# Performance work log

Measured on AMD Instinct MI355X. Metric: run time of the kernel, lower is better.

Reference implementation:

```python
import jax, jax.numpy as jnp
import numpy as np

B, T, I, H, O = 8192, 128, 28, 200, 10


def setup_inputs() -> dict:
    key = jax.random.key(0)
    ks = jax.random.split(key, 7)
    s_ih = 1.0 / np.sqrt(H)
    return {
        "x": jax.random.normal(ks[0], (B, T, I), dtype=jnp.float32),
        "W_ih": jax.random.uniform(ks[1], (H, I), jnp.float32, -s_ih, s_ih),
        "W_hh": jax.random.uniform(ks[2], (H, H), jnp.float32, -s_ih, s_ih),
        "b_ih": jax.random.uniform(ks[3], (H,), jnp.float32, -s_ih, s_ih),
        "b_hh": jax.random.uniform(ks[4], (H,), jnp.float32, -s_ih, s_ih),
        "W_fc": jax.random.uniform(ks[5], (O, H), jnp.float32, -s_ih, s_ih),
        "b_fc": jax.random.uniform(ks[6], (O,), jnp.float32, -s_ih, s_ih),
    }


def reference(x, W_ih, W_hh, b_ih, b_hh, W_fc, b_fc):
    # Precompute input projections for all timesteps in one GEMM: [B,T,H]
    xp = jnp.einsum("bti,hi->bth", x, W_ih) + b_ih + b_hh
    h0 = jnp.zeros((x.shape[0], W_hh.shape[0]), dtype=x.dtype)

    def step(h, xp_t):
        # h_t = relu(x_t W_ih^T + b_ih + h_{t-1} W_hh^T + b_hh)
        h = jax.nn.relu(xp_t + h @ W_hh.T)
        return h, None

    # scan over time: xp transposed to [T,B,H]
    h_last, _ = jax.lax.scan(step, h0, jnp.swapaxes(xp, 0, 1))
    # out[:, -1, :] then fc1
    return h_last @ W_fc.T + b_fc
```

## Files before the change

kernel.cpp:

```cpp
#include <hip/hip_runtime.h>

typedef float f4v __attribute__((ext_vector_type(4)));
typedef short s8v __attribute__((ext_vector_type(8)));

#define TT 128
#define II 28
#define HH 200
#define BB 16
#define NT 512
#define CH 8
#define KX 224
#define NCH (TT / CH)

template <bool B> struct BC { static constexpr bool value = B; };

__device__ __forceinline__ unsigned pk_hu(float a, float b) {
    unsigned ua = __builtin_bit_cast(unsigned, a) + 0x8000u;
    unsigned ub = __builtin_bit_cast(unsigned, b) + 0x8000u;
    return __builtin_amdgcn_perm(ub, ua, 0x07060302);
}
__device__ __forceinline__ short f2bf(float f) {
    return (short)((__builtin_bit_cast(unsigned, f) + 0x8000u) >> 16);
}
__device__ __forceinline__ float bf2f(short s) {
    return __builtin_bit_cast(float, ((unsigned)(unsigned short)s) << 16);
}

#define STEP_BAR() asm volatile("s_waitcnt lgkmcnt(0)\n\ts_barrier" ::: "memory")
#define VSTEP_BAR() asm volatile("s_waitcnt vmcnt(0) lgkmcnt(0)\n\ts_barrier" ::: "memory")

__global__ __launch_bounds__(NT, 4)
void rnn_r13(const float* __restrict__ x,
             const float* __restrict__ W_ih,
             const float* __restrict__ W_hh,
             const float* __restrict__ b_ih,
             const float* __restrict__ b_hh,
             const float* __restrict__ W_fc,
             const float* __restrict__ b_fc,
             float* __restrict__ out)
{
    __shared__ __align__(16) short Hf[2][7][512];
    __shared__ __align__(16) short Xf[2][CH][512];
    __shared__ __align__(16) float Xl[CH * BB * II];

    const int tid  = threadIdx.x;
    const int lane = tid & 63;
    const int q    = lane >> 4;
    const int lr   = lane & 15;
    const int wave = __builtin_amdgcn_readfirstlane(tid >> 6);
    const int b0   = blockIdx.x * BB;

    const bool two = (wave < 5);
    const int jt0  = two ? 2 * wave : 10 + (wave - 5);
    const int jt1  = two ? 2 * wave + 1 : 13;

    const int nIss = (wave < 6) ? 2 : 1;
    const int e0   = (wave < 6) ? 2 * wave : 12 + (wave - 6);
    unsigned xoff[2];
    #pragma unroll
    for (int k = 0; k < 2; ++k) {
        const int e  = e0 + k;
        const int m  = (e << 6) + lane;
        const int tl = m / 112;
        const int rm = m - tl * 112;
        const int r  = rm / 7;
        const int c4 = rm - r * 7;
        xoff[k] = (unsigned)(((((b0 + r) * TT + tl) * II) + c4 * 4) * 4);
    }
    auto issue_dma = [&](int c) {
        #pragma unroll
        for (int k = 0; k < 2; ++k) {
            if (k < nIss) {
                const char* src = (const char*)x + (xoff[k] + (unsigned)c * (CH * II * 4));
                float* dst = &Xl[(e0 + k) * 256];
                __builtin_amdgcn_global_load_lds(
                    (const __attribute__((address_space(1))) void*)src,
                    (__attribute__((address_space(3))) void*)dst, 16, 0, 0);
            }
        }
    };

    auto prepass = [&](int tc) {
        if (tid < 448) {
            const f4v v0 = *(const f4v*)&Xl[tid * 8];
            const f4v v1 = *(const f4v*)&Xl[tid * 8 + 4];
            const unsigned d[4] = { pk_hu(v0.x, v0.y), pk_hu(v0.z, v0.w),
                                    pk_hu(v1.x, v1.y), pk_hu(v1.z, v1.w) };
            int* dstb = ((int*)Xf) + (tc & 1) * 2048;
            #pragma unroll
            for (int dk = 0; dk < 4; ++dk) {
                const int kk = tid * 4 + dk;
                const int t  = kk / 224;
                const int k2 = kk - t * 224;
                const int r  = k2 / 14;
                const int cp = k2 - r * 14;
                dstb[t * 256 + 64 * (cp >> 2) + 4 * r + (cp & 3)] = (int)d[dk];
            }
        }
    };

    issue_dma(0);

    s8v Af[2][8];
    #pragma unroll
    for (int u = 0; u < 2; ++u) {
        const int j = 16 * (u ? jt1 : jt0) + lr;
        #pragma unroll
        for (int kc = 0; kc < 8; ++kc) {
            union { short s[8]; s8v v; } tv;
            #pragma unroll
            for (int i = 0; i < 8; ++i) {
                const int k = 32 * kc + 8 * q + i;
                float w = 0.0f;
                if (j < HH) {
                    if (k < HH)                     w = W_hh[j * HH + k];
                    else if (k >= KX && k < KX+II)  w = W_ih[j * II + (k - KX)];
                    else if (k == KX + II) {
                        w = b_ih[j] + b_hh[j];
                    } else if (k == KX + II + 1) {
                        const float bs = b_ih[j] + b_hh[j];
                        w = bs - bf2f(f2bf(bs));
                    }
                }
                tv.s[i] = f2bf(w);
            }
            Af[u][kc] = tv.v;
        }
    }

    for (int i = tid; i < 2 * 7 * 512 / 2; i += NT) ((int*)Hf)[i] = 0;
    for (int i = tid; i < 2 * CH * 512 / 2; i += NT)
        ((int*)Xf)[i] = (((i & 255) >= 194) && ((i & 3) == 2)) ? 0x3f803f80 : 0;

    const int j0w = 16 * jt0 + 4 * q;
    short* st0 = &Hf[0][j0w >> 5][(16 * ((j0w >> 3) & 3) + lr) * 8 + (j0w & 7)];
    const int j1w = 16 * jt1 + 4 * q;
    short* st1 = &Hf[0][j1w >> 5][(16 * ((j1w >> 3) & 3) + lr) * 8 + (j1w & 7)];
    const int HFH = 7 * 512;

    __syncthreads();
    prepass(0);
    STEP_BAR();
    issue_dma(1);

    if ((blockIdx.x >> 8) & 1) asm volatile("s_sleep 23");

    const f4v Z = {0.f, 0.f, 0.f, 0.f};
    f4v a0, a1;

    {
        const s8v xb = *(const s8v*)&Xf[0][0][lane * 8];
        a0 = __builtin_amdgcn_mfma_f32_16x16x32_bf16(Af[0][7], xb, Z, 0, 0, 0);
        if (two) a1 = __builtin_amdgcn_mfma_f32_16x16x32_bf16(Af[1][7], xb, Z, 0, 0, 0);
    }
    STEP_BAR();

    auto chunk = [&](int c, auto TWOC) {
        constexpr bool TWO = decltype(TWOC)::value;
        #pragma unroll
        for (int s = 0; s < CH; ++s) {
            const int pb = s & 1;
            const short* hf = &Hf[pb][0][lane * 8];
            if constexpr (TWO) {
                s8v g0 = *(const s8v*)(hf);
                s8v g1 = *(const s8v*)(hf + 512);
                s8v g2 = *(const s8v*)(hf + 1024);
                s8v g3 = *(const s8v*)(hf + 1536);
                a0 = __builtin_amdgcn_mfma_f32_16x16x32_bf16(Af[0][0], g0, a0, 0, 0, 0);
                a1 = __builtin_amdgcn_mfma_f32_16x16x32_bf16(Af[1][0], g0, a1, 0, 0, 0);
                g0 = *(const s8v*)(hf + 2048);
                a0 = __builtin_amdgcn_mfma_f32_16x16x32_bf16(Af[0][1], g1, a0, 0, 0, 0);
                a1 = __builtin_amdgcn_mfma_f32_16x16x32_bf16(Af[1][1], g1, a1, 0, 0, 0);
                g1 = *(const s8v*)(hf + 2560);
                a0 = __builtin_amdgcn_mfma_f32_16x16x32_bf16(Af[0][2], g2, a0, 0, 0, 0);
                a1 = __builtin_amdgcn_mfma_f32_16x16x32_bf16(Af[1][2], g2, a1, 0, 0, 0);
                g2 = *(const s8v*)(hf + 3072);
                a0 = __builtin_amdgcn_mfma_f32_16x16x32_bf16(Af[0][3], g3, a0, 0, 0, 0);
                a1 = __builtin_amdgcn_mfma_f32_16x16x32_bf16(Af[1][3], g3, a1, 0, 0, 0);
                a0 = __builtin_amdgcn_mfma_f32_16x16x32_bf16(Af[0][4], g0, a0, 0, 0, 0);
                a1 = __builtin_amdgcn_mfma_f32_16x16x32_bf16(Af[1][4], g0, a1, 0, 0, 0);
                a0 = __builtin_amdgcn_mfma_f32_16x16x32_bf16(Af[0][5], g1, a0, 0, 0, 0);
                a1 = __builtin_amdgcn_mfma_f32_16x16x32_bf16(Af[1][5], g1, a1, 0, 0, 0);
                a0 = __builtin_amdgcn_mfma_f32_16x16x32_bf16(Af[0][6], g2, a0, 0, 0, 0);
                a1 = __builtin_amdgcn_mfma_f32_16x16x32_bf16(Af[1][6], g2, a1, 0, 0, 0);
            } else {
                s8v g0 = *(const s8v*)(hf);
                s8v g1 = *(const s8v*)(hf + 1536);
                s8v g2 = *(const s8v*)(hf + 2048);
                s8v g3 = *(const s8v*)(hf + 2560);
                a1 = __builtin_amdgcn_mfma_f32_16x16x32_bf16(Af[0][3], g1, Z, 0, 0, 0);
                g1 = *(const s8v*)(hf + 512);
                a0 = __builtin_amdgcn_mfma_f32_16x16x32_bf16(Af[0][0], g0, a0, 0, 0, 0);
                g0 = *(const s8v*)(hf + 1024);
                a1 = __builtin_amdgcn_mfma_f32_16x16x32_bf16(Af[0][4], g2, a1, 0, 0, 0);
                g2 = *(const s8v*)(hf + 3072);
                a0 = __builtin_amdgcn_mfma_f32_16x16x32_bf16(Af[0][1], g1, a0, 0, 0, 0);
                a1 = __builtin_amdgcn_mfma_f32_16x16x32_bf16(Af[0][5], g3, a1, 0, 0, 0);
                a0 = __builtin_amdgcn_mfma_f32_16x16x32_bf16(Af[0][2], g0, a0, 0, 0, 0);
                a1 = __builtin_amdgcn_mfma_f32_16x16x32_bf16(Af[0][6], g2, a1, 0, 0, 0);
            }
            {
                const int wo = (pb ^ 1) * HFH;
                int2 hv;
                if constexpr (!TWO) a0 += a1;
                hv.x = (int)pk_hu(fmaxf(a0.x, 0.f), fmaxf(a0.y, 0.f));
                hv.y = (int)pk_hu(fmaxf(a0.z, 0.f), fmaxf(a0.w, 0.f));
                *(int2*)(st0 + wo) = hv;
                if constexpr (TWO) {
                    hv.x = (int)pk_hu(fmaxf(a1.x, 0.f), fmaxf(a1.y, 0.f));
                    hv.y = (int)pk_hu(fmaxf(a1.z, 0.f), fmaxf(a1.w, 0.f));
                    *(int2*)(st1 + wo) = hv;
                }
            }
            if (s < CH - 1) {
                const s8v xb = *(const s8v*)&Xf[c & 1][s + 1][lane * 8];
                a0 = __builtin_amdgcn_mfma_f32_16x16x32_bf16(Af[0][7], xb, Z, 0, 0, 0);
                if constexpr (TWO)
                    a1 = __builtin_amdgcn_mfma_f32_16x16x32_bf16(Af[1][7], xb, Z, 0, 0, 0);
            } else if (c + 1 < NCH) {
                const s8v xb = *(const s8v*)&Xf[(c + 1) & 1][0][lane * 8];
                a0 = __builtin_amdgcn_mfma_f32_16x16x32_bf16(Af[0][7], xb, Z, 0, 0, 0);
                if constexpr (TWO)
                    a1 = __builtin_amdgcn_mfma_f32_16x16x32_bf16(Af[1][7], xb, Z, 0, 0, 0);
            }
            if (s == 4 && c + 1 < NCH) prepass(c + 1);
            if (s == 5 && c + 2 < NCH) issue_dma(c + 2);
            if (s == 3) VSTEP_BAR();
            else        STEP_BAR();
        }
    };

    #pragma unroll 1
    for (int c = 0; c < NCH; ++c) {
        if (two) chunk(c, BC<true>{});
        else     chunk(c, BC<false>{});
    }

    __syncthreads();
    if (tid < BB * 10) {
        const int o = tid >> 4, r = tid & 15;
        const float* wrow = W_fc + o * HH;
        float acc = b_fc[o];
        #pragma unroll 1
        for (int kb = 0; kb < 25; ++kb) {
            const s8v hv = *(const s8v*)&Hf[0][kb >> 2][(16 * (kb & 3) + r) * 8];
            const f4v w0 = *(const f4v*)(wrow + kb * 8);
            const f4v w1 = *(const f4v*)(wrow + kb * 8 + 4);
            acc = fmaf(bf2f(hv[0]), w0.x, acc);
            acc = fmaf(bf2f(hv[1]), w0.y, acc);
            acc = fmaf(bf2f(hv[2]), w0.z, acc);
            acc = fmaf(bf2f(hv[3]), w0.w, acc);
            acc = fmaf(bf2f(hv[4]), w1.x, acc);
            acc = fmaf(bf2f(hv[5]), w1.y, acc);
            acc = fmaf(bf2f(hv[6]), w1.z, acc);
            acc = fmaf(bf2f(hv[7]), w1.w, acc);
        }
        __builtin_nontemporal_store(acc, &out[(long)(b0 + r) * 10 + o]);
    }
}

extern "C" void kernel_launch(void* const* d_in, const int* in_sizes, int n_in,
                              void* d_out, int out_size, void* d_ws, size_t ws_size,
                              hipStream_t stream) {
    const float* x    = (const float*)d_in[0];
    const float* W_ih = (const float*)d_in[1];
    const float* W_hh = (const float*)d_in[2];
    const float* b_ih = (const float*)d_in[3];
    const float* b_hh = (const float*)d_in[4];
    const float* W_fc = (const float*)d_in[5];
    const float* b_fc = (const float*)d_in[6];
    float* out = (float*)d_out;

    rnn_r13<<<dim3(8192 / BB), dim3(NT), 0, stream>>>(
        x, W_ih, W_hh, b_ih, b_hh, W_fc, b_fc, out);
}
```

Measured before the change: 277.4 us.

## Rotate wave roles per block, drop s_sleep stagger, pin MFMA/LDS schedule

The wave-to-tile assignment is rotated by two for every other group of 256 blocks, so the waves holding two tiles differ between co-resident blocks. This replaces the earlier s_sleep stagger meant to desynchronise blocks sharing a CU. The two-tile path now keeps three LDS fragment registers instead of four and uses sched_group_barrier to interleave ds_reads with MFMAs. The aim is to spread MFMA pressure across SIMDs and hide LDS latency inside the recurrent step. It risks scheduler constraints that conflict with the compiler's own order, and bank or SIMD imbalance from the rotated mapping.

```diff
diff --git a/kernel.cpp b/kernel.cpp
--- a/kernel.cpp
+++ b/kernel.cpp
@@ -29,8 +29,11 @@
 #define STEP_BAR() asm volatile("s_waitcnt lgkmcnt(0)\n\ts_barrier" ::: "memory")
 #define VSTEP_BAR() asm volatile("s_waitcnt vmcnt(0) lgkmcnt(0)\n\ts_barrier" ::: "memory")
 
+#define MFMA16(d, A, g, Cin) d = __builtin_amdgcn_mfma_f32_16x16x32_bf16(A, g, Cin, 0, 0, 0)
+#define SGB __builtin_amdgcn_sched_group_barrier
+
 __global__ __launch_bounds__(NT, 4)
-void rnn_r13(const float* __restrict__ x,
+void rnn_r15(const float* __restrict__ x,
              const float* __restrict__ W_ih,
              const float* __restrict__ W_hh,
              const float* __restrict__ b_ih,
@@ -50,9 +53,10 @@
     const int wave = __builtin_amdgcn_readfirstlane(tid >> 6);
     const int b0   = blockIdx.x * BB;
 
-    const bool two = (wave < 5);
-    const int jt0  = two ? 2 * wave : 10 + (wave - 5);
-    const int jt1  = two ? 2 * wave + 1 : 13;
+    const int wrot = (wave + 2 * ((blockIdx.x >> 8) & 1)) & 7;
+    const bool two = (wrot < 5);
+    const int jt0  = two ? 2 * wrot : 10 + (wrot - 5);
+    const int jt1  = two ? 2 * wrot + 1 : 13;
 
     const int nIss = (wave < 6) ? 2 : 1;
     const int e0   = (wave < 6) ? 2 * wave : 12 + (wave - 6);
@@ -143,15 +147,13 @@
     STEP_BAR();
     issue_dma(1);
 
-    if ((blockIdx.x >> 8) & 1) asm volatile("s_sleep 23");
-
     const f4v Z = {0.f, 0.f, 0.f, 0.f};
     f4v a0, a1;
 
     {
         const s8v xb = *(const s8v*)&Xf[0][0][lane * 8];
-        a0 = __builtin_amdgcn_mfma_f32_16x16x32_bf16(Af[0][7], xb, Z, 0, 0, 0);
-        if (two) a1 = __builtin_amdgcn_mfma_f32_16x16x32_bf16(Af[1][7], xb, Z, 0, 0, 0);
+        MFMA16(a0, Af[0][7], xb, Z);
+        if (two) MFMA16(a1, Af[1][7], xb, Z);
     }
     STEP_BAR();
 
@@ -165,39 +167,46 @@
                 s8v g0 = *(const s8v*)(hf);
                 s8v g1 = *(const s8v*)(hf + 512);
                 s8v g2 = *(const s8v*)(hf + 1024);
-                s8v g3 = *(const s8v*)(hf + 1536);
-                a0 = __builtin_amdgcn_mfma_f32_16x16x32_bf16(Af[0][0], g0, a0, 0, 0, 0);
-                a1 = __builtin_amdgcn_mfma_f32_16x16x32_bf16(Af[1][0], g0, a1, 0, 0, 0);
-                g0 = *(const s8v*)(hf + 2048);
-                a0 = __builtin_amdgcn_mfma_f32_16x16x32_bf16(Af[0][1], g1, a0, 0, 0, 0);
-                a1 = __builtin_amdgcn_mfma_f32_16x16x32_bf16(Af[1][1], g1, a1, 0, 0, 0);
-                g1 = *(const s8v*)(hf + 2560);
-                a0 = __builtin_amdgcn_mfma_f32_16x16x32_bf16(Af[0][2], g2, a0, 0, 0, 0);
-                a1 = __builtin_amdgcn_mfma_f32_16x16x32_bf16(Af[1][2], g2, a1, 0, 0, 0);
-                g2 = *(const s8v*)(hf + 3072);
-                a0 = __builtin_amdgcn_mfma_f32_16x16x32_bf16(Af[0][3], g3, a0, 0, 0, 0);
-                a1 = __builtin_amdgcn_mfma_f32_16x16x32_bf16(Af[1][3], g3, a1, 0, 0, 0);
-                a0 = __builtin_amdgcn_mfma_f32_16x16x32_bf16(Af[0][4], g0, a0, 0, 0, 0);
-                a1 = __builtin_amdgcn_mfma_f32_16x16x32_bf16(Af[1][4], g0, a1, 0, 0, 0);
-                a0 = __builtin_amdgcn_mfma_f32_16x16x32_bf16(Af[0][5], g1, a0, 0, 0, 0);
-                a1 = __builtin_amdgcn_mfma_f32_16x16x32_bf16(Af[1][5], g1, a1, 0, 0, 0);
-                a0 = __builtin_amdgcn_mfma_f32_16x16x32_bf16(Af[0][6], g2, a0, 0, 0, 0);
-                a1 = __builtin_amdgcn_mfma_f32_16x16x32_bf16(Af[1][6], g2, a1, 0, 0, 0);
+                MFMA16(a0, Af[0][0], g0, a0);
+                MFMA16(a1, Af[1][0], g0, a1);
+                g0 = *(const s8v*)(hf + 1536);
+                MFMA16(a0, Af[0][1], g1, a0);
+                MFMA16(a1, Af[1][1], g1, a1);
+                g1 = *(const s8v*)(hf + 2048);
+                MFMA16(a0, Af[0][2], g2, a0);
+                MFMA16(a1, Af[1][2], g2, a1);
+                g2 = *(const s8v*)(hf + 2560);
+                MFMA16(a0, Af[0][3], g0, a0);
+                MFMA16(a1, Af[1][3], g0, a1);
+                g0 = *(const s8v*)(hf + 3072);
+                MFMA16(a0, Af[0][4], g1, a0);
+                MFMA16(a1, Af[1][4], g1, a1);
+                MFMA16(a0, Af[0][5], g2, a0);
+                MFMA16(a1, Af[1][5], g2, a1);
+                MFMA16(a0, Af[0][6], g0, a0);
+                MFMA16(a1, Af[1][6], g0, a1);
+                SGB(0x100, 2, 0);
+                SGB(0x100, 1, 0); SGB(0x8, 2, 0);
+                SGB(0x100, 1, 0); SGB(0x8, 2, 0);
+                SGB(0x100, 1, 0); SGB(0x8, 2, 0);
+                SGB(0x100, 1, 0); SGB(0x8, 2, 0);
+                SGB(0x100, 1, 0); SGB(0x8, 2, 0);
+                SGB(0x8, 2, 0); SGB(0x8, 2, 0);
             } else {
                 s8v g0 = *(const s8v*)(hf);
                 s8v g1 = *(const s8v*)(hf + 1536);
                 s8v g2 = *(const s8v*)(hf + 2048);
                 s8v g3 = *(const s8v*)(hf + 2560);
-                a1 = __builtin_amdgcn_mfma_f32_16x16x32_bf16(Af[0][3], g1, Z, 0, 0, 0);
+                MFMA16(a1, Af[0][3], g1, Z);
                 g1 = *(const s8v*)(hf + 512);
-                a0 = __builtin_amdgcn_mfma_f32_16x16x32_bf16(Af[0][0], g0, a0, 0, 0, 0);
+                MFMA16(a0, Af[0][0], g0, a0);
                 g0 = *(const s8v*)(hf + 1024);
-                a1 = __builtin_amdgcn_mfma_f32_16x16x32_bf16(Af[0][4], g2, a1, 0, 0, 0);
+                MFMA16(a1, Af[0][4], g2, a1);
                 g2 = *(const s8v*)(hf + 3072);
-                a0 = __builtin_amdgcn_mfma_f32_16x16x32_bf16(Af[0][1], g1, a0, 0, 0, 0);
-                a1 = __builtin_amdgcn_mfma_f32_16x16x32_bf16(Af[0][5], g3, a1, 0, 0, 0);
-                a0 = __builtin_amdgcn_mfma_f32_16x16x32_bf16(Af[0][2], g0, a0, 0, 0, 0);
-                a1 = __builtin_amdgcn_mfma_f32_16x16x32_bf16(Af[0][6], g2, a1, 0, 0, 0);
+                MFMA16(a0, Af[0][1], g1, a0);
+                MFMA16(a1, Af[0][5], g3, a1);
+                MFMA16(a0, Af[0][2], g0, a0);
+                MFMA16(a1, Af[0][6], g2, a1);
             }
             {
                 const int wo = (pb ^ 1) * HFH;
@@ -214,14 +223,12 @@
             }
             if (s < CH - 1) {
                 const s8v xb = *(const s8v*)&Xf[c & 1][s + 1][lane * 8];
-                a0 = __builtin_amdgcn_mfma_f32_16x16x32_bf16(Af[0][7], xb, Z, 0, 0, 0);
-                if constexpr (TWO)
-                    a1 = __builtin_amdgcn_mfma_f32_16x16x32_bf16(Af[1][7], xb, Z, 0, 0, 0);
+                MFMA16(a0, Af[0][7], xb, Z);
+                if constexpr (TWO) MFMA16(a1, Af[1][7], xb, Z);
             } else if (c + 1 < NCH) {
                 const s8v xb = *(const s8v*)&Xf[(c + 1) & 1][0][lane * 8];
-                a0 = __builtin_amdgcn_mfma_f32_16x16x32_bf16(Af[0][7], xb, Z, 0, 0, 0);
-                if constexpr (TWO)
-                    a1 = __builtin_amdgcn_mfma_f32_16x16x32_bf16(Af[1][7], xb, Z, 0, 0, 0);
+                MFMA16(a0, Af[0][7], xb, Z);
+                if constexpr (TWO) MFMA16(a1, Af[1][7], xb, Z);
             }
             if (s == 4 && c + 1 < NCH) prepass(c + 1);
             if (s == 5 && c + 2 < NCH) issue_dma(c + 2);
@@ -271,6 +278,6 @@
     const float* b_fc = (const float*)d_in[6];
     float* out = (float*)d_out;
 
-    rnn_r13<<<dim3(8192 / BB), dim3(NT), 0, stream>>>(
+    rnn_r15<<<dim3(8192 / BB), dim3(NT), 0, stream>>>(
         x, W_ih, W_hh, b_ih, b_hh, W_fc, b_fc, out);
 }
```

Result: no change. 277.3 us (-0.0%).
